# Kernel optimization log

Measured on AMD Instinct MI355X. Metric: run time of the kernel, lower is better.

## Reference

```python
import jax, jax.numpy as jnp
import numpy as np

N = 100000      # nodes
E = 1600000     # edges (avg degree 16)
IN, H, H4, OUT = 2, 128, 32, 64
B = 1000        # batch_size for final view


def setup_inputs() -> dict:
    key = jax.random.key(0)
    ks = jax.random.split(key, 16)
    w = lambda k, s: (jax.random.normal(k, s, jnp.float32) * (1.0 / np.sqrt(s[0])))
    return {
        "x": jax.random.normal(ks[0], (N, IN), jnp.float32),
        "edge_index": jax.random.randint(ks[1], (2, E), 0, N, dtype=jnp.int32),
        "batch_size": B,
        "W1": w(ks[2], (IN, H)),  "b1": jnp.zeros((H,), jnp.float32),
        "W2": w(ks[3], (H, H)),   "b2": jnp.zeros((H,), jnp.float32),
        "W3": w(ks[4], (H, H4)),  "b3": jnp.zeros((H4,), jnp.float32),
        "W4": w(ks[5], (H4, H4)), "b4": jnp.zeros((H4,), jnp.float32),
        "W5": w(ks[6], (H4, OUT)),"b5": jnp.zeros((OUT,), jnp.float32),
        "Wl": w(ks[7], (OUT, 1)), "bl": jnp.zeros((1,), jnp.float32),
    }


def gcn_conv(x, src, dst, W, b, n):
    # PyG GCNConv: add self-loops, symmetric degree normalization, scatter-add.
    h = x @ W  # [N, F]
    deg = jax.ops.segment_sum(jnp.ones(src.shape[0], h.dtype), dst,
                              num_segments=n) + 1.0  # +1 for self-loop
    dinv = jax.lax.rsqrt(deg)  # deg >= 1, no inf
    norm = dinv[src] * dinv[dst]  # [E]
    agg = jax.ops.segment_sum(h[src] * norm[:, None], dst, num_segments=n)
    agg = agg + h * (dinv * dinv)[:, None]  # self-loop contribution
    return agg + b


def reference(x, edge_index, batch_size, W1, b1, W2, b2, W3, b3, W4, b4, W5, b5, Wl, bl):
    x = x.reshape(-1, 2)
    n = x.shape[0]
    src, dst = edge_index[0], edge_index[1]
    for W, b in ((W1, b1), (W2, b2), (W3, b3), (W4, b4), (W5, b5)):
        x = jax.nn.relu(gcn_conv(x, src, dst, W, b, n))
    x = x @ Wl + bl  # [N, 1]
    return x.reshape(batch_size, -1)
```

## Files before the change

kernel.cpp:

```cpp
#include <hip/hip_runtime.h>
#include <math.h>


static inline int cdiv(int a, int b) { return (a + b - 1) / b; }

__global__ void zero_i32(int* __restrict__ p, int n) {
    int i = blockIdx.x * 256 + threadIdx.x;
    if (i < n) p[i] = 0;
}

__global__ void count_kernel(const int* __restrict__ dst, int* __restrict__ cnt, int E) {
    int e = blockIdx.x * 256 + threadIdx.x;
    if (e < E) atomicAdd(&cnt[dst[e]], 1);
}

__global__ void scan1(const int* __restrict__ cnt, int* __restrict__ off,
                      int* __restrict__ bsum, int n) {
    __shared__ int sm[256];
    int i = blockIdx.x * 256 + threadIdx.x;
    int v = (i < n) ? cnt[i] : 0;
    sm[threadIdx.x] = v;
    __syncthreads();
    for (int ofs = 1; ofs < 256; ofs <<= 1) {
        int t = (threadIdx.x >= (unsigned)ofs) ? sm[threadIdx.x - ofs] : 0;
        __syncthreads();
        sm[threadIdx.x] += t;
        __syncthreads();
    }
    if (i < n) off[i] = sm[threadIdx.x];
    if (threadIdx.x == 255) bsum[blockIdx.x] = sm[255];
}

__global__ void scan2(const int* __restrict__ bsum, int* __restrict__ bpre,
                      int nb, int* __restrict__ off, int N, int E) {
    __shared__ int sm[512];
    int t = threadIdx.x;
    sm[t] = (t < nb) ? bsum[t] : 0;
    __syncthreads();
    for (int ofs = 1; ofs < 512; ofs <<= 1) {
        int v = (t >= ofs) ? sm[t - ofs] : 0;
        __syncthreads();
        sm[t] += v;
        __syncthreads();
    }
    if (t < nb) bpre[t] = sm[t] - bsum[t];
    if (t == 0) off[N] = E;
}

__global__ void scan3_fused(const int* __restrict__ cnt, const int* __restrict__ bpre,
                            int* __restrict__ off, int* __restrict__ cursor,
                            const float* __restrict__ x, float* __restrict__ dinv,
                            float* __restrict__ xs, int n) {
    int i = blockIdx.x * 256 + threadIdx.x;
    if (i < n) {
        int c = cnt[i];
        int o = off[i] - c + bpre[blockIdx.x];
        off[i] = o;
        cursor[i] = o;
        float dv = 1.0f / sqrtf((float)c + 1.0f);
        dinv[i] = dv;
        float2 xv = *reinterpret_cast<const float2*>(x + 2 * (size_t)i);
        *reinterpret_cast<float2*>(xs + 2 * (size_t)i) = float2{dv * xv.x, dv * xv.y};
    }
}

__global__ __launch_bounds__(256) void fill_ranged(const int* __restrict__ src,
                                                   const int* __restrict__ dst,
                                                   int* __restrict__ cursor,
                                                   int* __restrict__ csr,
                                                   int E, int N, int echunk) {
    int cls = blockIdx.x & 7;
    int chunk = blockIdx.x >> 3;
    int per = (N + 7) >> 3;
    int lo = cls * per;
    int hi = lo + per; if (hi > N) hi = N;
    int e0 = chunk * echunk;
    int e1 = e0 + echunk; if (e1 > E) e1 = E;
    for (int e = e0 + (int)threadIdx.x; e < e1; e += 256) {
        int d = dst[e];
        if (d >= lo && d < hi) {
            int p = atomicAdd(&cursor[d], 1);
            csr[p] = src[e];
        }
    }
}

__global__ __launch_bounds__(256) void agg2_kernel(const float* __restrict__ xs,
                                                   const int* __restrict__ off,
                                                   const int* __restrict__ csr,
                                                   const float* __restrict__ dinv,
                                                   float* __restrict__ out, int n) {
    int v = blockIdx.x * 256 + threadIdx.x;
    if (v >= n) return;
    float a0 = 0.f, a1 = 0.f;
    int e0 = off[v], e1 = off[v + 1];
    for (int e = e0; e < e1; e++) {
        int s = csr[e];
        float2 q = *reinterpret_cast<const float2*>(xs + 2 * (size_t)s);
        a0 += q.x;
        a1 += q.y;
    }
    float dv = dinv[v];
    float2 xv = *reinterpret_cast<const float2*>(xs + 2 * (size_t)v);
    *reinterpret_cast<float2*>(out + 2 * (size_t)v) =
        float2{dv * (a0 + xv.x), dv * (a1 + xv.y)};
}

template <bool BR, bool PS>
__global__ __launch_bounds__(256) void agg128_kernel(const float* __restrict__ h,
                                                     const int* __restrict__ off,
                                                     const int* __restrict__ csr,
                                                     const float* __restrict__ dinv,
                                                     const float* __restrict__ bias,
                                                     float* __restrict__ out, int n) {
    int tid = threadIdx.x;
    int lane = tid & 63;
    int sl = lane & 15;
    int subbase = lane & ~15;
    int wave = tid >> 6;
    int v = blockIdx.x * 16 + wave * 4 + (lane >> 4);
    if (v >= n) return;

    int start = off[v];
    int end = off[v + 1];

    float4 accA = {0.f, 0.f, 0.f, 0.f};
    float4 accB = {0.f, 0.f, 0.f, 0.f};

    for (int base = start; base < end; base += 16) {
        int m = end - base;
        if (m > 16) m = 16;
        int idx = (sl < m) ? csr[base + sl] : 0;
        int i = 0;
        for (; i + 8 <= m; i += 8) {
            float4 ha[8], hb[8];
#pragma unroll
            for (int u = 0; u < 8; u++) {
                int s = __shfl(idx, subbase + i + u);
                const float* p = h + (size_t)s * 128 + sl * 8;
                ha[u] = *reinterpret_cast<const float4*>(p);
                hb[u] = *reinterpret_cast<const float4*>(p + 4);
            }
#pragma unroll
            for (int u = 0; u < 8; u++) {
                accA.x += ha[u].x; accA.y += ha[u].y; accA.z += ha[u].z; accA.w += ha[u].w;
                accB.x += hb[u].x; accB.y += hb[u].y; accB.z += hb[u].z; accB.w += hb[u].w;
            }
        }
        if (i + 4 <= m) {
            float4 ha[4], hb[4];
#pragma unroll
            for (int u = 0; u < 4; u++) {
                int s = __shfl(idx, subbase + i + u);
                const float* p = h + (size_t)s * 128 + sl * 8;
                ha[u] = *reinterpret_cast<const float4*>(p);
                hb[u] = *reinterpret_cast<const float4*>(p + 4);
            }
#pragma unroll
            for (int u = 0; u < 4; u++) {
                accA.x += ha[u].x; accA.y += ha[u].y; accA.z += ha[u].z; accA.w += ha[u].w;
                accB.x += hb[u].x; accB.y += hb[u].y; accB.z += hb[u].z; accB.w += hb[u].w;
            }
            i += 4;
        }
        if (i + 2 <= m) {
            int s0 = __shfl(idx, subbase + i);
            int s1 = __shfl(idx, subbase + i + 1);
            const float* p0 = h + (size_t)s0 * 128 + sl * 8;
            const float* p1 = h + (size_t)s1 * 128 + sl * 8;
            float4 a0 = *reinterpret_cast<const float4*>(p0);
            float4 b0 = *reinterpret_cast<const float4*>(p0 + 4);
            float4 a1 = *reinterpret_cast<const float4*>(p1);
            float4 b1 = *reinterpret_cast<const float4*>(p1 + 4);
            accA.x += a0.x + a1.x; accA.y += a0.y + a1.y;
            accA.z += a0.z + a1.z; accA.w += a0.w + a1.w;
            accB.x += b0.x + b1.x; accB.y += b0.y + b1.y;
            accB.z += b0.z + b1.z; accB.w += b0.w + b1.w;
            i += 2;
        }
        if (i < m) {
            int s0 = __shfl(idx, subbase + i);
            const float* p0 = h + (size_t)s0 * 128 + sl * 8;
            float4 a0 = *reinterpret_cast<const float4*>(p0);
            float4 b0 = *reinterpret_cast<const float4*>(p0 + 4);
            accA.x += a0.x; accA.y += a0.y; accA.z += a0.z; accA.w += a0.w;
            accB.x += b0.x; accB.y += b0.y; accB.z += b0.z; accB.w += b0.w;
        }
    }

    float dv = dinv[v];
    const float* pv = h + (size_t)v * 128 + sl * 8;
    float4 hvA = *reinterpret_cast<const float4*>(pv);
    float4 hvB = *reinterpret_cast<const float4*>(pv + 4);
    float4 oA, oB;
    oA.x = dv * (accA.x + hvA.x); oA.y = dv * (accA.y + hvA.y);
    oA.z = dv * (accA.z + hvA.z); oA.w = dv * (accA.w + hvA.w);
    oB.x = dv * (accB.x + hvB.x); oB.y = dv * (accB.y + hvB.y);
    oB.z = dv * (accB.z + hvB.z); oB.w = dv * (accB.w + hvB.w);
    if constexpr (BR) {
        float4 bA = *reinterpret_cast<const float4*>(bias + sl * 8);
        float4 bB = *reinterpret_cast<const float4*>(bias + sl * 8 + 4);
        oA.x = fmaxf(oA.x + bA.x, 0.f); oA.y = fmaxf(oA.y + bA.y, 0.f);
        oA.z = fmaxf(oA.z + bA.z, 0.f); oA.w = fmaxf(oA.w + bA.w, 0.f);
        oB.x = fmaxf(oB.x + bB.x, 0.f); oB.y = fmaxf(oB.y + bB.y, 0.f);
        oB.z = fmaxf(oB.z + bB.z, 0.f); oB.w = fmaxf(oB.w + bB.w, 0.f);
    }
    if constexpr (PS) {
        oA.x *= dv; oA.y *= dv; oA.z *= dv; oA.w *= dv;
        oB.x *= dv; oB.y *= dv; oB.z *= dv; oB.w *= dv;
    }
    float* po = out + (size_t)v * 128 + sl * 8;
    *reinterpret_cast<float4*>(po) = oA;
    *reinterpret_cast<float4*>(po + 4) = oB;
}

template <bool BR, bool PS>
__global__ __launch_bounds__(256) void agg32_kernel(const float* __restrict__ h,
                                                    const int* __restrict__ off,
                                                    const int* __restrict__ csr,
                                                    const float* __restrict__ dinv,
                                                    const float* __restrict__ bias,
                                                    float* __restrict__ out, int n) {
    int tid = threadIdx.x;
    int lane = tid & 63;
    int sl = lane & 7;
    int subbase = lane & ~7;
    int wave = tid >> 6;
    int v = blockIdx.x * 32 + wave * 8 + (lane >> 3);
    if (v >= n) return;

    int start = off[v];
    int end = off[v + 1];

    float4 acc = {0.f, 0.f, 0.f, 0.f};

    for (int base = start; base < end; base += 16) {
        int m = end - base;
        if (m > 16) m = 16;
        int idxA = (sl < m) ? csr[base + sl] : 0;
        int idxB = (8 + sl < m) ? csr[base + 8 + sl] : 0;
        if (m == 16) {
            float4 hb[16];
#pragma unroll
            for (int u = 0; u < 16; u++) {
                int s = __shfl((u < 8) ? idxA : idxB, subbase + (u & 7));
                hb[u] = *reinterpret_cast<const float4*>(h + (size_t)s * 32 + sl * 4);
            }
#pragma unroll
            for (int u = 0; u < 16; u++) {
                acc.x += hb[u].x; acc.y += hb[u].y; acc.z += hb[u].z; acc.w += hb[u].w;
            }
        } else {
            int ma = (m < 8) ? m : 8;
            int i = 0;
            for (; i + 4 <= ma; i += 4) {
                float4 hb[4];
#pragma unroll
                for (int u = 0; u < 4; u++) {
                    int s = __shfl(idxA, subbase + i + u);
                    hb[u] = *reinterpret_cast<const float4*>(h + (size_t)s * 32 + sl * 4);
                }
#pragma unroll
                for (int u = 0; u < 4; u++) {
                    acc.x += hb[u].x; acc.y += hb[u].y; acc.z += hb[u].z; acc.w += hb[u].w;
                }
            }
            if (i + 2 <= ma) {
                int s0 = __shfl(idxA, subbase + i);
                int s1 = __shfl(idxA, subbase + i + 1);
                float4 h0 = *reinterpret_cast<const float4*>(h + (size_t)s0 * 32 + sl * 4);
                float4 h1 = *reinterpret_cast<const float4*>(h + (size_t)s1 * 32 + sl * 4);
                acc.x += h0.x + h1.x; acc.y += h0.y + h1.y;
                acc.z += h0.z + h1.z; acc.w += h0.w + h1.w;
                i += 2;
            }
            if (i < ma) {
                int s0 = __shfl(idxA, subbase + i);
                float4 h0 = *reinterpret_cast<const float4*>(h + (size_t)s0 * 32 + sl * 4);
                acc.x += h0.x; acc.y += h0.y; acc.z += h0.z; acc.w += h0.w;
            }
            if (m > 8) {
                int mb = m - 8;
                int j = 0;
                for (; j + 4 <= mb; j += 4) {
                    float4 hb[4];
#pragma unroll
                    for (int u = 0; u < 4; u++) {
                        int s = __shfl(idxB, subbase + j + u);
                        hb[u] = *reinterpret_cast<const float4*>(h + (size_t)s * 32 + sl * 4);
                    }
#pragma unroll
                    for (int u = 0; u < 4; u++) {
                        acc.x += hb[u].x; acc.y += hb[u].y; acc.z += hb[u].z; acc.w += hb[u].w;
                    }
                }
                if (j + 2 <= mb) {
                    int s0 = __shfl(idxB, subbase + j);
                    int s1 = __shfl(idxB, subbase + j + 1);
                    float4 h0 = *reinterpret_cast<const float4*>(h + (size_t)s0 * 32 + sl * 4);
                    float4 h1 = *reinterpret_cast<const float4*>(h + (size_t)s1 * 32 + sl * 4);
                    acc.x += h0.x + h1.x; acc.y += h0.y + h1.y;
                    acc.z += h0.z + h1.z; acc.w += h0.w + h1.w;
                    j += 2;
                }
                if (j < mb) {
                    int s0 = __shfl(idxB, subbase + j);
                    float4 h0 = *reinterpret_cast<const float4*>(h + (size_t)s0 * 32 + sl * 4);
                    acc.x += h0.x; acc.y += h0.y; acc.z += h0.z; acc.w += h0.w;
                }
            }
        }
    }

    float dv = dinv[v];
    float4 hv = *reinterpret_cast<const float4*>(h + (size_t)v * 32 + sl * 4);
    float o0 = dv * (acc.x + hv.x);
    float o1 = dv * (acc.y + hv.y);
    float o2 = dv * (acc.z + hv.z);
    float o3 = dv * (acc.w + hv.w);
    if constexpr (BR) {
        float4 b = *reinterpret_cast<const float4*>(bias + sl * 4);
        o0 = fmaxf(o0 + b.x, 0.f);
        o1 = fmaxf(o1 + b.y, 0.f);
        o2 = fmaxf(o2 + b.z, 0.f);
        o3 = fmaxf(o3 + b.w, 0.f);
    }
    if constexpr (PS) {
        o0 *= dv; o1 *= dv; o2 *= dv; o3 *= dv;
    }
    *reinterpret_cast<float4*>(out + (size_t)v * 32 + sl * 4) = float4{o0, o1, o2, o3};
}

template <int K, int F, bool BR, bool PS>
__global__ __launch_bounds__(256, 4) void gemm_tiled(const float* __restrict__ x,
                                                     const float* __restrict__ W,
                                                     const float* __restrict__ bias,
                                                     const float* __restrict__ dinv,
                                                     float* __restrict__ h, int n) {
    constexpr int KC = 32;
    constexpr int KCP = 36;
    constexpr int ROWS = 64;
    constexpr int TPC = F / 4;
    constexpr int RT = 256 / TPC;
    constexpr int RPT = ROWS / RT;
    static_assert(K % KC == 0, "K must be a multiple of 32");

    __shared__ float Ws[KC * F];
    __shared__ float Xs[ROWS * KCP];

    const int tid = threadIdx.x;
    const int cb = (tid % TPC) * 4;
    const int tr = tid / TPC;
    const int row0 = blockIdx.x * ROWS;

    float acc[RPT][4];
#pragma unroll
    for (int r = 0; r < RPT; r++)
#pragma unroll
        for (int j = 0; j < 4; j++) acc[r][j] = 0.f;

#pragma unroll 1
    for (int k0 = 0; k0 < K; k0 += KC) {
        __syncthreads();
        {
            int r = tid >> 2;
            int kk = (tid & 3) * 8;
            int gr = row0 + r;
            float4 v0 = {0.f, 0.f, 0.f, 0.f}, v1 = {0.f, 0.f, 0.f, 0.f};
            if (gr < n) {
                v0 = *reinterpret_cast<const float4*>(x + (size_t)gr * K + k0 + kk);
                v1 = *reinterpret_cast<const float4*>(x + (size_t)gr * K + k0 + kk + 4);
            }
            *reinterpret_cast<float4*>(&Xs[r * KCP + kk]) = v0;
            *reinterpret_cast<float4*>(&Xs[r * KCP + kk + 4]) = v1;
        }
        for (int i = tid; i < KC * F / 4; i += 256) {
            *reinterpret_cast<float4*>(&Ws[i * 4]) =
                *reinterpret_cast<const float4*>(W + (size_t)k0 * F + i * 4);
        }
        __syncthreads();

#pragma unroll 4
        for (int kk4 = 0; kk4 < KC; kk4 += 4) {
            float4 xr[RPT];
#pragma unroll
            for (int r = 0; r < RPT; r++)
                xr[r] = *reinterpret_cast<const float4*>(&Xs[(tr * RPT + r) * KCP + kk4]);
#pragma unroll
            for (int j = 0; j < 4; j++) {
                float4 w = *reinterpret_cast<const float4*>(&Ws[(kk4 + j) * F + cb]);
#pragma unroll
                for (int r = 0; r < RPT; r++) {
                    float xv = (j == 0) ? xr[r].x : (j == 1) ? xr[r].y
                             : (j == 2) ? xr[r].z : xr[r].w;
                    acc[r][0] += xv * w.x;
                    acc[r][1] += xv * w.y;
                    acc[r][2] += xv * w.z;
                    acc[r][3] += xv * w.w;
                }
            }
        }
    }

    float4 b = float4{0.f, 0.f, 0.f, 0.f};
    if constexpr (BR) b = *reinterpret_cast<const float4*>(bias + cb);
#pragma unroll
    for (int r = 0; r < RPT; r++) {
        int row = row0 + tr * RPT + r;
        if (row < n) {
            float o0 = acc[r][0], o1 = acc[r][1], o2 = acc[r][2], o3 = acc[r][3];
            if constexpr (BR) {
                o0 = fmaxf(o0 + b.x, 0.f);
                o1 = fmaxf(o1 + b.y, 0.f);
                o2 = fmaxf(o2 + b.z, 0.f);
                o3 = fmaxf(o3 + b.w, 0.f);
            }
            if constexpr (PS) {
                float dv = dinv[row];
                o0 *= dv; o1 *= dv; o2 *= dv; o3 *= dv;
            }
            *reinterpret_cast<float4*>(&h[(size_t)row * F + cb]) = float4{o0, o1, o2, o3};
        }
    }
}

__global__ __launch_bounds__(256, 4) void gemm_final(const float* __restrict__ x,
                                                     const float* __restrict__ W,
                                                     const float* __restrict__ bias,
                                                     const float* __restrict__ Wl,
                                                     const float* __restrict__ bl,
                                                     float* __restrict__ out, int n) {
    constexpr int K = 32, F = 64;
    constexpr int KC = 32;
    constexpr int KCP = 36;
    constexpr int ROWS = 64;
    constexpr int TPC = F / 4;
    constexpr int RT = 256 / TPC;
    constexpr int RPT = ROWS / RT;

    __shared__ float Ws[KC * F];
    __shared__ float Xs[ROWS * KCP];
    __shared__ float wl[F];

    const int tid = threadIdx.x;
    if (tid < F) wl[tid] = Wl[tid];
    const int cb = (tid % TPC) * 4;
    const int tr = tid / TPC;
    const int row0 = blockIdx.x * ROWS;

    float acc[RPT][4];
#pragma unroll
    for (int r = 0; r < RPT; r++)
#pragma unroll
        for (int j = 0; j < 4; j++) acc[r][j] = 0.f;

    {
        {
            int r = tid >> 2;
            int kk = (tid & 3) * 8;
            int gr = row0 + r;
            float4 v0 = {0.f, 0.f, 0.f, 0.f}, v1 = {0.f, 0.f, 0.f, 0.f};
            if (gr < n) {
                v0 = *reinterpret_cast<const float4*>(x + (size_t)gr * K + kk);
                v1 = *reinterpret_cast<const float4*>(x + (size_t)gr * K + kk + 4);
            }
            *reinterpret_cast<float4*>(&Xs[r * KCP + kk]) = v0;
            *reinterpret_cast<float4*>(&Xs[r * KCP + kk + 4]) = v1;
        }
        for (int i = tid; i < KC * F / 4; i += 256) {
            *reinterpret_cast<float4*>(&Ws[i * 4]) =
                *reinterpret_cast<const float4*>(W + i * 4);
        }
        __syncthreads();

#pragma unroll 4
        for (int kk4 = 0; kk4 < KC; kk4 += 4) {
            float4 xr[RPT];
#pragma unroll
            for (int r = 0; r < RPT; r++)
                xr[r] = *reinterpret_cast<const float4*>(&Xs[(tr * RPT + r) * KCP + kk4]);
#pragma unroll
            for (int j = 0; j < 4; j++) {
                float4 w = *reinterpret_cast<const float4*>(&Ws[(kk4 + j) * F + cb]);
#pragma unroll
                for (int r = 0; r < RPT; r++) {
                    float xv = (j == 0) ? xr[r].x : (j == 1) ? xr[r].y
                             : (j == 2) ? xr[r].z : xr[r].w;
                    acc[r][0] += xv * w.x;
                    acc[r][1] += xv * w.y;
                    acc[r][2] += xv * w.z;
                    acc[r][3] += xv * w.w;
                }
            }
        }
    }

    float4 b = *reinterpret_cast<const float4*>(bias + cb);
    float4 w = *reinterpret_cast<const float4*>(&wl[cb]);
    float blv = bl[0];
#pragma unroll
    for (int r = 0; r < RPT; r++) {
        int row = row0 + tr * RPT + r;
        float o0 = fmaxf(acc[r][0] + b.x, 0.f);
        float o1 = fmaxf(acc[r][1] + b.y, 0.f);
        float o2 = fmaxf(acc[r][2] + b.z, 0.f);
        float o3 = fmaxf(acc[r][3] + b.w, 0.f);
        float partial = o0 * w.x + o1 * w.y + o2 * w.z + o3 * w.w;
        partial += __shfl_xor(partial, 8, 16);
        partial += __shfl_xor(partial, 4, 16);
        partial += __shfl_xor(partial, 2, 16);
        partial += __shfl_xor(partial, 1, 16);
        if ((tid & 15) == 0 && row < n) out[row] = partial + blv;
    }
}

template <int K, int F, bool BR, bool PS>
__global__ __launch_bounds__(256, 4) void gemm_small(const float* __restrict__ x,
                                                     const float* __restrict__ W,
                                                     const float* __restrict__ bias,
                                                     const float* __restrict__ dinv,
                                                     float* __restrict__ h, int n) {
    constexpr int TPR = F / 4;
    constexpr int ROWS = 256 / TPR;
    __shared__ float Ws[K * F];
    for (int i = threadIdx.x; i < K * F; i += 256) Ws[i] = W[i];
    __syncthreads();

    int tid = threadIdx.x;
    int cb = (tid % TPR) * 4;
    int r = blockIdx.x * ROWS + tid / TPR;
    if (r >= n) return;

    const float* xr = x + (size_t)r * K;
    float a0 = 0.f, a1 = 0.f, a2 = 0.f, a3 = 0.f;
#pragma unroll
    for (int k = 0; k < K; k++) {
        float xv = xr[k];
        float4 w = *reinterpret_cast<const float4*>(&Ws[k * F + cb]);
        a0 += xv * w.x; a1 += xv * w.y; a2 += xv * w.z; a3 += xv * w.w;
    }
    if constexpr (BR) {
        float4 b = *reinterpret_cast<const float4*>(bias + cb);
        a0 = fmaxf(a0 + b.x, 0.f);
        a1 = fmaxf(a1 + b.y, 0.f);
        a2 = fmaxf(a2 + b.z, 0.f);
        a3 = fmaxf(a3 + b.w, 0.f);
    }
    if constexpr (PS) {
        float dv = dinv[r];
        a0 *= dv; a1 *= dv; a2 *= dv; a3 *= dv;
    }
    *reinterpret_cast<float4*>(&h[(size_t)r * F + cb]) = float4{a0, a1, a2, a3};
}

extern "C" void kernel_launch(void* const* d_in, const int* in_sizes, int n_in,
                              void* d_out, int out_size, void* d_ws, size_t ws_size,
                              hipStream_t stream) {
    const float* x = (const float*)d_in[0];
    const int* ei = (const int*)d_in[1];
    const float* W1 = (const float*)d_in[3];
    const float* b1 = (const float*)d_in[4];
    const float* W2 = (const float*)d_in[5];
    const float* b2 = (const float*)d_in[6];
    const float* W3 = (const float*)d_in[7];
    const float* b3 = (const float*)d_in[8];
    const float* W4 = (const float*)d_in[9];
    const float* b4 = (const float*)d_in[10];
    const float* W5 = (const float*)d_in[11];
    const float* b5 = (const float*)d_in[12];
    const float* Wl = (const float*)d_in[13];
    const float* bl = (const float*)d_in[14];

    const int N = in_sizes[0] / 2;
    const int E = in_sizes[1] / 2;
    const int* src = ei;
    const int* dst = ei + E;

    char* wp = (char*)d_ws;
    auto alloc = [&](size_t bytes) -> void* {
        void* p = wp;
        wp += ((bytes + 255) / 256) * 256;
        return p;
    };
    int* cnt = (int*)alloc((size_t)N * 4);
    int* off = (int*)alloc((size_t)(N + 1) * 4);
    int* cursor = (int*)alloc((size_t)N * 4);
    int* bsum = (int*)alloc(512 * 4);
    int* bpre = (int*)alloc(512 * 4);
    int* csr = (int*)alloc((size_t)E * 4);
    float* dinv = (float*)alloc((size_t)N * 4);
    float* xs2 = (float*)alloc((size_t)N * 2 * 4);
    float* t2 = (float*)alloc((size_t)N * 2 * 4);
    float* bufA = (float*)alloc((size_t)N * 128 * 4);
    float* bufB = (float*)alloc((size_t)N * 128 * 4);

    const int gN = cdiv(N, 256);
    const int gE = cdiv(E, 256);
    const int nb = gN;
    const int gT = cdiv(N, 64);

    const int NCHUNK = 128;
    const int echunk = cdiv(E, NCHUNK);
    const int gR = 8 * NCHUNK;

    zero_i32<<<gN, 256, 0, stream>>>(cnt, N);
    count_kernel<<<gE, 256, 0, stream>>>(dst, cnt, E);
    scan1<<<nb, 256, 0, stream>>>(cnt, off, bsum, N);
    scan2<<<1, 512, 0, stream>>>(bsum, bpre, nb, off, N, E);
    scan3_fused<<<nb, 256, 0, stream>>>(cnt, bpre, off, cursor, x, dinv, xs2, N);
    fill_ranged<<<gR, 256, 0, stream>>>(src, dst, cursor, csr, E, N, echunk);

    agg2_kernel<<<gN, 256, 0, stream>>>(xs2, off, csr, dinv, t2, N);
    gemm_small<2, 128, true, true><<<cdiv(N, 8), 256, 0, stream>>>(t2, W1, b1, dinv, bufA, N);
    gemm_tiled<128, 128, false, false><<<gT, 256, 0, stream>>>(bufA, W2, nullptr, nullptr, bufB, N);
    agg128_kernel<true, true><<<cdiv(N, 16), 256, 0, stream>>>(bufB, off, csr, dinv, b2, bufA, N);
    gemm_tiled<128, 32, false, false><<<gT, 256, 0, stream>>>(bufA, W3, nullptr, nullptr, bufB, N);
    agg32_kernel<true, true><<<cdiv(N, 32), 256, 0, stream>>>(bufB, off, csr, dinv, b3, bufA, N);
    gemm_tiled<32, 32, false, false><<<gT, 256, 0, stream>>>(bufA, W4, nullptr, nullptr, bufB, N);
    agg32_kernel<true, true><<<cdiv(N, 32), 256, 0, stream>>>(bufB, off, csr, dinv, b4, bufA, N);
    agg32_kernel<false, false><<<cdiv(N, 32), 256, 0, stream>>>(bufA, off, csr, dinv, nullptr, bufB, N);
    gemm_final<<<gT, 256, 0, stream>>>(bufB, W5, b5, Wl, bl, (float*)d_out, N);
}
```

Before: 564.1 us.

## Split 128-wide features into 32-column chunk planes for cache-friendly aggregation

The layer-2 GEMM now writes its 128-wide output as four separate [N,32] column-chunk planes. The aggregation kernel processes one chunk and one half of the nodes per block class, and the next GEMM reads the chunked layout back. The aim is to shrink the gather working set (each plane is about 12.8MB) so random neighbor reads hit in L2 or the MALL instead of DRAM. The cost is more blocks and more index loads, since the CSR is re-read once per chunk, and 128-byte gathers that are less efficient per access.

```diff
diff --git a/kernel.cpp b/kernel.cpp
--- a/kernel.cpp
+++ b/kernel.cpp
@@ -107,111 +107,130 @@
 }
 
 template <bool BR, bool PS>
-__global__ __launch_bounds__(256) void agg128_kernel(const float* __restrict__ h,
-                                                     const int* __restrict__ off,
-                                                     const int* __restrict__ csr,
-                                                     const float* __restrict__ dinv,
-                                                     const float* __restrict__ bias,
-                                                     float* __restrict__ out, int n) {
+__global__ __launch_bounds__(256) void agg128x_kernel(const float* __restrict__ hc,
+                                                      const int* __restrict__ off,
+                                                      const int* __restrict__ csr,
+                                                      const float* __restrict__ dinv,
+                                                      const float* __restrict__ bias,
+                                                      float* __restrict__ outc, int n) {
+    int cls = blockIdx.x & 7;
+    int chunk = cls >> 1;
+    int half = cls & 1;
+    int n2 = (n + 1) >> 1;
+    int lo = half * n2;
+    int hi = lo + n2; if (hi > n) hi = n;
+
+    const float* __restrict__ h = hc + (size_t)chunk * n * 32;
+    float* __restrict__ out = outc + (size_t)chunk * n * 32;
+
     int tid = threadIdx.x;
     int lane = tid & 63;
-    int sl = lane & 15;
-    int subbase = lane & ~15;
+    int sl = lane & 7;
+    int subbase = lane & ~7;
     int wave = tid >> 6;
-    int v = blockIdx.x * 16 + wave * 4 + (lane >> 4);
-    if (v >= n) return;
+    int v = lo + (blockIdx.x >> 3) * 32 + wave * 8 + (lane >> 3);
+    if (v >= hi) return;
 
     int start = off[v];
     int end = off[v + 1];
 
-    float4 accA = {0.f, 0.f, 0.f, 0.f};
-    float4 accB = {0.f, 0.f, 0.f, 0.f};
+    float4 acc = {0.f, 0.f, 0.f, 0.f};
 
     for (int base = start; base < end; base += 16) {
         int m = end - base;
         if (m > 16) m = 16;
-        int idx = (sl < m) ? csr[base + sl] : 0;
-        int i = 0;
-        for (; i + 8 <= m; i += 8) {
-            float4 ha[8], hb[8];
-#pragma unroll
-            for (int u = 0; u < 8; u++) {
-                int s = __shfl(idx, subbase + i + u);
-                const float* p = h + (size_t)s * 128 + sl * 8;
-                ha[u] = *reinterpret_cast<const float4*>(p);
-                hb[u] = *reinterpret_cast<const float4*>(p + 4);
-            }
-#pragma unroll
-            for (int u = 0; u < 8; u++) {
-                accA.x += ha[u].x; accA.y += ha[u].y; accA.z += ha[u].z; accA.w += ha[u].w;
-                accB.x += hb[u].x; accB.y += hb[u].y; accB.z += hb[u].z; accB.w += hb[u].w;
-            }
-        }
-        if (i + 4 <= m) {
-            float4 ha[4], hb[4];
-#pragma unroll
-            for (int u = 0; u < 4; u++) {
-                int s = __shfl(idx, subbase + i + u);
-                const float* p = h + (size_t)s * 128 + sl * 8;
-                ha[u] = *reinterpret_cast<const float4*>(p);
-                hb[u] = *reinterpret_cast<const float4*>(p + 4);
-            }
-#pragma unroll
-            for (int u = 0; u < 4; u++) {
-                accA.x += ha[u].x; accA.y += ha[u].y; accA.z += ha[u].z; accA.w += ha[u].w;
-                accB.x += hb[u].x; accB.y += hb[u].y; accB.z += hb[u].z; accB.w += hb[u].w;
-            }
-            i += 4;
-        }
-        if (i + 2 <= m) {
-            int s0 = __shfl(idx, subbase + i);
-            int s1 = __shfl(idx, subbase + i + 1);
-            const float* p0 = h + (size_t)s0 * 128 + sl * 8;
-            const float* p1 = h + (size_t)s1 * 128 + sl * 8;
-            float4 a0 = *reinterpret_cast<const float4*>(p0);
-            float4 b0 = *reinterpret_cast<const float4*>(p0 + 4);
-            float4 a1 = *reinterpret_cast<const float4*>(p1);
-            float4 b1 = *reinterpret_cast<const float4*>(p1 + 4);
-            accA.x += a0.x + a1.x; accA.y += a0.y + a1.y;
-            accA.z += a0.z + a1.z; accA.w += a0.w + a1.w;
-            accB.x += b0.x + b1.x; accB.y += b0.y + b1.y;
-            accB.z += b0.z + b1.z; accB.w += b0.w + b1.w;
-            i += 2;
-        }
-        if (i < m) {
-            int s0 = __shfl(idx, subbase + i);
-            const float* p0 = h + (size_t)s0 * 128 + sl * 8;
-            float4 a0 = *reinterpret_cast<const float4*>(p0);
-            float4 b0 = *reinterpret_cast<const float4*>(p0 + 4);
-            accA.x += a0.x; accA.y += a0.y; accA.z += a0.z; accA.w += a0.w;
-            accB.x += b0.x; accB.y += b0.y; accB.z += b0.z; accB.w += b0.w;
+        int idxA = (sl < m) ? csr[base + sl] : 0;
+        int idxB = (8 + sl < m) ? csr[base + 8 + sl] : 0;
+        if (m == 16) {
+            float4 hb[16];
+#pragma unroll
+            for (int u = 0; u < 16; u++) {
+                int s = __shfl((u < 8) ? idxA : idxB, subbase + (u & 7));
+                hb[u] = *reinterpret_cast<const float4*>(h + (size_t)s * 32 + sl * 4);
+            }
+#pragma unroll
+            for (int u = 0; u < 16; u++) {
+                acc.x += hb[u].x; acc.y += hb[u].y; acc.z += hb[u].z; acc.w += hb[u].w;
+            }
+        } else {
+            int ma = (m < 8) ? m : 8;
+            int i = 0;
+            for (; i + 4 <= ma; i += 4) {
+                float4 hb[4];
+#pragma unroll
+                for (int u = 0; u < 4; u++) {
+                    int s = __shfl(idxA, subbase + i + u);
+                    hb[u] = *reinterpret_cast<const float4*>(h + (size_t)s * 32 + sl * 4);
+                }
+#pragma unroll
+                for (int u = 0; u < 4; u++) {
+                    acc.x += hb[u].x; acc.y += hb[u].y; acc.z += hb[u].z; acc.w += hb[u].w;
+                }
+            }
+            if (i + 2 <= ma) {
+                int s0 = __shfl(idxA, subbase + i);
+                int s1 = __shfl(idxA, subbase + i + 1);
+                float4 h0 = *reinterpret_cast<const float4*>(h + (size_t)s0 * 32 + sl * 4);
+                float4 h1 = *reinterpret_cast<const float4*>(h + (size_t)s1 * 32 + sl * 4);
+                acc.x += h0.x + h1.x; acc.y += h0.y + h1.y;
+                acc.z += h0.z + h1.z; acc.w += h0.w + h1.w;
+                i += 2;
+            }
+            if (i < ma) {
+                int s0 = __shfl(idxA, subbase + i);
+                float4 h0 = *reinterpret_cast<const float4*>(h + (size_t)s0 * 32 + sl * 4);
+                acc.x += h0.x; acc.y += h0.y; acc.z += h0.z; acc.w += h0.w;
+            }
+            if (m > 8) {
+                int mb = m - 8;
+                int j = 0;
+                for (; j + 4 <= mb; j += 4) {
+                    float4 hb[4];
+#pragma unroll
+                    for (int u = 0; u < 4; u++) {
+                        int s = __shfl(idxB, subbase + j + u);
+                        hb[u] = *reinterpret_cast<const float4*>(h + (size_t)s * 32 + sl * 4);
+                    }
+#pragma unroll
+                    for (int u = 0; u < 4; u++) {
+                        acc.x += hb[u].x; acc.y += hb[u].y; acc.z += hb[u].z; acc.w += hb[u].w;
+                    }
+                }
+                if (j + 2 <= mb) {
+                    int s0 = __shfl(idxB, subbase + j);
+                    int s1 = __shfl(idxB, subbase + j + 1);
+                    float4 h0 = *reinterpret_cast<const float4*>(h + (size_t)s0 * 32 + sl * 4);
+                    float4 h1 = *reinterpret_cast<const float4*>(h + (size_t)s1 * 32 + sl * 4);
+                    acc.x += h0.x + h1.x; acc.y += h0.y + h1.y;
+                    acc.z += h0.z + h1.z; acc.w += h0.w + h1.w;
+                    j += 2;
+                }
+                if (j < mb) {
+                    int s0 = __shfl(idxB, subbase + j);
+                    float4 h0 = *reinterpret_cast<const float4*>(h + (size_t)s0 * 32 + sl * 4);
+                    acc.x += h0.x; acc.y += h0.y; acc.z += h0.z; acc.w += h0.w;
+                }
+            }
         }
     }
 
     float dv = dinv[v];
-    const float* pv = h + (size_t)v * 128 + sl * 8;
-    float4 hvA = *reinterpret_cast<const float4*>(pv);
-    float4 hvB = *reinterpret_cast<const float4*>(pv + 4);
-    float4 oA, oB;
-    oA.x = dv * (accA.x + hvA.x); oA.y = dv * (accA.y + hvA.y);
-    oA.z = dv * (accA.z + hvA.z); oA.w = dv * (accA.w + hvA.w);
-    oB.x = dv * (accB.x + hvB.x); oB.y = dv * (accB.y + hvB.y);
-    oB.z = dv * (accB.z + hvB.z); oB.w = dv * (accB.w + hvB.w);
+    float4 hv = *reinterpret_cast<const float4*>(h + (size_t)v * 32 + sl * 4);
+    float o0 = dv * (acc.x + hv.x);
+    float o1 = dv * (acc.y + hv.y);
+    float o2 = dv * (acc.z + hv.z);
+    float o3 = dv * (acc.w + hv.w);
     if constexpr (BR) {
-        float4 bA = *reinterpret_cast<const float4*>(bias + sl * 8);
-        float4 bB = *reinterpret_cast<const float4*>(bias + sl * 8 + 4);
-        oA.x = fmaxf(oA.x + bA.x, 0.f); oA.y = fmaxf(oA.y + bA.y, 0.f);
-        oA.z = fmaxf(oA.z + bA.z, 0.f); oA.w = fmaxf(oA.w + bA.w, 0.f);
-        oB.x = fmaxf(oB.x + bB.x, 0.f); oB.y = fmaxf(oB.y + bB.y, 0.f);
-        oB.z = fmaxf(oB.z + bB.z, 0.f); oB.w = fmaxf(oB.w + bB.w, 0.f);
+        float4 b = *reinterpret_cast<const float4*>(bias + chunk * 32 + sl * 4);
+        o0 = fmaxf(o0 + b.x, 0.f);
+        o1 = fmaxf(o1 + b.y, 0.f);
+        o2 = fmaxf(o2 + b.z, 0.f);
+        o3 = fmaxf(o3 + b.w, 0.f);
     }
     if constexpr (PS) {
-        oA.x *= dv; oA.y *= dv; oA.z *= dv; oA.w *= dv;
-        oB.x *= dv; oB.y *= dv; oB.z *= dv; oB.w *= dv;
-    }
-    float* po = out + (size_t)v * 128 + sl * 8;
-    *reinterpret_cast<float4*>(po) = oA;
-    *reinterpret_cast<float4*>(po + 4) = oB;
+        o0 *= dv; o1 *= dv; o2 *= dv; o3 *= dv;
+    }
+    *reinterpret_cast<float4*>(out + (size_t)v * 32 + sl * 4) = float4{o0, o1, o2, o3};
 }
 
 template <bool BR, bool PS>
@@ -331,7 +350,7 @@
     *reinterpret_cast<float4*>(out + (size_t)v * 32 + sl * 4) = float4{o0, o1, o2, o3};
 }
 
-template <int K, int F, bool BR, bool PS>
+template <int K, int F, bool BR, bool PS, int CIN = 0, int COUT = 0>
 __global__ __launch_bounds__(256, 4) void gemm_tiled(const float* __restrict__ x,
                                                      const float* __restrict__ W,
                                                      const float* __restrict__ bias,
@@ -368,8 +387,14 @@
             int gr = row0 + r;
             float4 v0 = {0.f, 0.f, 0.f, 0.f}, v1 = {0.f, 0.f, 0.f, 0.f};
             if (gr < n) {
-                v0 = *reinterpret_cast<const float4*>(x + (size_t)gr * K + k0 + kk);
-                v1 = *reinterpret_cast<const float4*>(x + (size_t)gr * K + k0 + kk + 4);
+                if constexpr (CIN == 32) {
+                    const float* xb = x + (size_t)(k0 >> 5) * n * 32 + (size_t)gr * 32 + kk;
+                    v0 = *reinterpret_cast<const float4*>(xb);
+                    v1 = *reinterpret_cast<const float4*>(xb + 4);
+                } else {
+                    v0 = *reinterpret_cast<const float4*>(x + (size_t)gr * K + k0 + kk);
+                    v1 = *reinterpret_cast<const float4*>(x + (size_t)gr * K + k0 + kk + 4);
+                }
             }
             *reinterpret_cast<float4*>(&Xs[r * KCP + kk]) = v0;
             *reinterpret_cast<float4*>(&Xs[r * KCP + kk + 4]) = v1;
@@ -419,7 +444,12 @@
                 float dv = dinv[row];
                 o0 *= dv; o1 *= dv; o2 *= dv; o3 *= dv;
             }
-            *reinterpret_cast<float4*>(&h[(size_t)row * F + cb]) = float4{o0, o1, o2, o3};
+            if constexpr (COUT == 32) {
+                float* hb = h + (size_t)(cb >> 5) * n * 32 + (size_t)row * 32 + (cb & 31);
+                *reinterpret_cast<float4*>(hb) = float4{o0, o1, o2, o3};
+            } else {
+                *reinterpret_cast<float4*>(&h[(size_t)row * F + cb]) = float4{o0, o1, o2, o3};
+            }
         }
     }
 }
@@ -603,6 +633,8 @@
     const int echunk = cdiv(E, NCHUNK);
     const int gR = 8 * NCHUNK;
 
+    const int gX = 8 * cdiv((N + 1) / 2, 32);
+
     zero_i32<<<gN, 256, 0, stream>>>(cnt, N);
     count_kernel<<<gE, 256, 0, stream>>>(dst, cnt, E);
     scan1<<<nb, 256, 0, stream>>>(cnt, off, bsum, N);
@@ -612,11 +644,11 @@
 
     agg2_kernel<<<gN, 256, 0, stream>>>(xs2, off, csr, dinv, t2, N);
     gemm_small<2, 128, true, true><<<cdiv(N, 8), 256, 0, stream>>>(t2, W1, b1, dinv, bufA, N);
-    gemm_tiled<128, 128, false, false><<<gT, 256, 0, stream>>>(bufA, W2, nullptr, nullptr, bufB, N);
-    agg128_kernel<true, true><<<cdiv(N, 16), 256, 0, stream>>>(bufB, off, csr, dinv, b2, bufA, N);
-    gemm_tiled<128, 32, false, false><<<gT, 256, 0, stream>>>(bufA, W3, nullptr, nullptr, bufB, N);
+    gemm_tiled<128, 128, false, false, 0, 32><<<gT, 256, 0, stream>>>(bufA, W2, nullptr, nullptr, bufB, N);
+    agg128x_kernel<true, true><<<gX, 256, 0, stream>>>(bufB, off, csr, dinv, b2, bufA, N);
+    gemm_tiled<128, 32, false, false, 32, 0><<<gT, 256, 0, stream>>>(bufA, W3, nullptr, nullptr, bufB, N);
     agg32_kernel<true, true><<<cdiv(N, 32), 256, 0, stream>>>(bufB, off, csr, dinv, b3, bufA, N);
-    gemm_tiled<32, 32, false, false><<<gT, 256, 0, stream>>>(bufA, W4, nullptr, nullptr, bufB, N);
+    gemm_tiled<32, 32, false, false, 0, 0><<<gT, 256, 0, stream>>>(bufA, W4, nullptr, nullptr, bufB, N);
     agg32_kernel<true, true><<<cdiv(N, 32), 256, 0, stream>>>(bufB, off, csr, dinv, b4, bufA, N);
     agg32_kernel<false, false><<<cdiv(N, 32), 256, 0, stream>>>(bufA, off, csr, dinv, nullptr, bufB, N);
     gemm_final<<<gT, 256, 0, stream>>>(bufB, W5, b5, Wl, bl, (float*)d_out, N);
```

Result: faster. 530.5 us (-6.0%).
